# Performance work log

Measured on AMD Instinct MI355X. Metric: run time of the kernel, lower is better.

## Reference

```python
import jax, jax.numpy as jnp
import numpy as np

B, N, C, F, O = 32, 2048, 8, 128, 128


def setup_inputs() -> dict:
    key = jax.random.key(0)
    k1, k2, k3, k4, k5, k6 = jax.random.split(key, 6)
    nodes = jax.random.normal(k1, (B, N, F), dtype=jnp.float32)
    children = jax.random.randint(k2, (B, N, C), 0, N, dtype=jnp.int32)
    w_t = jax.random.normal(k3, (F, O), dtype=jnp.float32) * 0.05
    w_l = jax.random.normal(k4, (F, O), dtype=jnp.float32) * 0.05
    w_r = jax.random.normal(k5, (F, O), dtype=jnp.float32) * 0.05
    b = jax.random.normal(k6, (O,), dtype=jnp.float32) * 0.05
    return {"nodes": nodes, "children": children, "w_t": w_t, "w_l": w_l, "w_r": w_r, "b": b}


def reference(nodes, children, w_t, w_l, w_r, b):
    Bb, Nn, Ff = nodes.shape
    Cc = children.shape[2]
    dt = nodes.dtype

    # --- children tensor: index 0 maps to zero vector ---
    lookup = jnp.concatenate([jnp.zeros((Bb, 1, Ff), dt), nodes[:, 1:, :]], axis=1)
    batch_idx = jnp.arange(Bb)[:, None, None]
    child_vecs = lookup[batch_idx, children]                      # [B,N,C,F]
    tree = jnp.concatenate([nodes[:, :, None, :], child_vecs], axis=2)  # [B,N,C+1,F]

    # --- coefficients ---
    ch_f = children.astype(dt)
    c_t = jnp.broadcast_to(
        jnp.concatenate([jnp.ones((1, 1, 1), dt), jnp.zeros((1, 1, Cc), dt)], axis=2),
        (Bb, Nn, Cc + 1))                                          # [B,N,C+1]
    num_sib = jnp.count_nonzero(children, axis=2, keepdims=True).astype(dt)  # [B,N,1]
    mask = jnp.concatenate(
        [jnp.zeros((Bb, Nn, 1), dt), jnp.minimum(ch_f, 1.0)], axis=2)        # [B,N,C+1]
    child_indices = jnp.arange(-1.0, Cc, 1.0, dtype=dt)[None, None, :] * mask
    singles = jnp.concatenate(
        [jnp.zeros((Bb, Nn, 1), dt),
         jnp.full((Bb, Nn, 1), 0.5, dt),
         jnp.zeros((Bb, Nn, Cc - 1), dt)], axis=2)
    is_single = num_sib == 1.0
    denom = jnp.where(is_single, 1.0, num_sib - 1.0)  # safe divide, matches tf.where select
    c_r = jnp.where(is_single, singles, (1.0 - c_t) * (child_indices / denom))
    c_l = (1.0 - c_t) * (1.0 - c_r) * mask
    coef = jnp.stack([c_t, c_r, c_l], axis=3)                      # [B,N,C+1,3]

    # --- weighted aggregation + small GEMM ---
    agg = jnp.einsum('bncf,bnck->bnkf', tree, coef)                # [B,N,3,F]
    w = jnp.stack([w_t, w_r, w_l], axis=0)                         # [3,F,O]
    out = jnp.einsum('bnkf,kfo->bno', agg, w)
    return jax.nn.relu(out + b)
```

## Files before the change

### kernel.cpp

```cpp
#include <hip/hip_runtime.h>

typedef unsigned short ushort_t;
typedef __attribute__((ext_vector_type(8))) short short8;
typedef __attribute__((ext_vector_type(4))) short short4v;
typedef __attribute__((ext_vector_type(4))) float float4v;

#define Bn 32
#define Nn 2048
#define Cn 8
#define Fn 128
#define On 128
#define Kn 384
#define MT 16
#define LDSK 392

__device__ __forceinline__ ushort_t f2bf(float x) {
  unsigned u = __float_as_uint(x);
  u += 0x7fffu + ((u >> 16) & 1u);
  return (ushort_t)(u >> 16);
}

__global__ void prep_w_kernel(const float* __restrict__ w_t,
                              const float* __restrict__ w_l,
                              const float* __restrict__ w_r,
                              ushort_t* __restrict__ wsw) {
  int t = blockIdx.x * blockDim.x + threadIdx.x;
  if (t >= 6144) return;
  int lane = t & 63;
  int r = t >> 6;
  int ks = r % 12;
  int q = r / 12;
  int col = q * 16 + (lane & 15);
  int kbase = ((lane >> 4) * 8) + ks * 32;
  ushort_t* dst = wsw + (size_t)t * 8;
#pragma unroll
  for (int j = 0; j < 8; ++j) {
    int k = kbase + j;
    const float* src = (k < Fn) ? w_t : (k < 2 * Fn) ? w_r : w_l;
    int f = k & (Fn - 1);
    dst[j] = f2bf(src[f * On + col]);
  }
}

__global__ __launch_bounds__(128, 5)
void tree_conv_kernel(const float* __restrict__ nodes,
                      const int* __restrict__ children,
                      const ushort_t* __restrict__ wsw,
                      const float* __restrict__ bias,
                      float* __restrict__ out) {
  __shared__ __align__(16) ushort_t agg[MT * LDSK];

  const int tid = threadIdx.x;

  const int sb = ((blockIdx.x & 7) << 9) | (blockIdx.x >> 3);

  {
    const int grp = tid >> 5;
    const int ln = tid & 31;

    int4 ca[4], cb[4];
#pragma unroll
    for (int it = 0; it < 4; ++it) {
      const int g = sb * MT + it * 4 + grp;
      const int4* chv = (const int4*)(children + (size_t)g * Cn);
      ca[it] = chv[0];
      cb[it] = chv[1];
    }

#pragma unroll
    for (int it = 0; it < 4; ++it) {
      const int row = it * 4 + grp;
      const int g = sb * MT + row;
      const int base_row = g & ~(Nn - 1);

      int idx[Cn] = {ca[it].x, ca[it].y, ca[it].z, ca[it].w,
                     cb[it].x, cb[it].y, cb[it].z, cb[it].w};

      int ns = 0;
#pragma unroll
      for (int c = 0; c < Cn; ++c) ns += (idx[c] != 0);
      const float denom = (ns > 1) ? (float)(ns - 1) : 1.0f;

      float crv[Cn], clv[Cn];
#pragma unroll
      for (int c = 0; c < Cn; ++c) {
        float m = (idx[c] != 0) ? 1.0f : 0.0f;
        float cr0 = (ns == 1) ? ((c == 0) ? 0.5f : 0.0f) : ((float)c / denom);
        float cr = cr0 * m;
        crv[c] = cr;
        clv[c] = (1.0f - cr) * m;
        idx[c] &= (Nn - 1);
      }

      const float4v sv = *((const float4v*)(nodes + (size_t)g * Fn) + ln);

      float4v rr = {0.f, 0.f, 0.f, 0.f};
      float4v ll = {0.f, 0.f, 0.f, 0.f};
#pragma unroll
      for (int c = 0; c < Cn; ++c) {
        const float4v v =
            *((const float4v*)(nodes + (size_t)(base_row + idx[c]) * Fn) + ln);
        rr += crv[c] * v;
        ll += clv[c] * v;
      }

      ushort_t* arow = agg + row * LDSK;
      short4v ps = {(short)f2bf(sv.x), (short)f2bf(sv.y),
                    (short)f2bf(sv.z), (short)f2bf(sv.w)};
      short4v pr = {(short)f2bf(rr.x), (short)f2bf(rr.y),
                    (short)f2bf(rr.z), (short)f2bf(rr.w)};
      short4v pl = {(short)f2bf(ll.x), (short)f2bf(ll.y),
                    (short)f2bf(ll.z), (short)f2bf(ll.w)};
      *(short4v*)(arow + ln * 4) = ps;
      *(short4v*)(arow + Fn + ln * 4) = pr;
      *(short4v*)(arow + 2 * Fn + ln * 4) = pl;
    }
  }

  __syncthreads();

  const int lane = tid & 63;
  const int wave = tid >> 6;
  const int l15 = lane & 15;
  const int quad = lane >> 4;

#pragma unroll
  for (int ct = 0; ct < 4; ++ct) {
    const int q = wave * 4 + ct;
    const short8* bp = (const short8*)wsw + (q * 12) * 64 + lane;
    short8 bfrag[12];
#pragma unroll
    for (int ks = 0; ks < 12; ++ks) bfrag[ks] = bp[ks * 64];

    const int col = q * 16 + l15;
    const float bb = bias[col];

    const ushort_t* ar = agg + l15 * LDSK + quad * 8;
    float4v acc = {0.f, 0.f, 0.f, 0.f};
#pragma unroll
    for (int ks = 0; ks < 12; ++ks) {
      short8 af = *(const short8*)(ar + ks * 32);
      acc = __builtin_amdgcn_mfma_f32_16x16x32_bf16(af, bfrag[ks], acc, 0, 0, 0);
    }
    const int grow0 = sb * MT + quad * 4;
#pragma unroll
    for (int r2 = 0; r2 < 4; ++r2) {
      out[(size_t)(grow0 + r2) * On + col] = fmaxf(acc[r2] + bb, 0.f);
    }
  }
}

extern "C" void kernel_launch(void* const* d_in, const int* in_sizes, int n_in,
                              void* d_out, int out_size, void* d_ws, size_t ws_size,
                              hipStream_t stream) {
  const float* nodes = (const float*)d_in[0];
  const int* children = (const int*)d_in[1];
  const float* w_t = (const float*)d_in[2];
  const float* w_l = (const float*)d_in[3];
  const float* w_r = (const float*)d_in[4];
  const float* bias = (const float*)d_in[5];
  float* out = (float*)d_out;
  ushort_t* wsw = (ushort_t*)d_ws;

  prep_w_kernel<<<24, 256, 0, stream>>>(w_t, w_l, w_r, wsw);
  tree_conv_kernel<<<(Bn * Nn) / MT, 128, 0, stream>>>(nodes, children, wsw, bias, out);
}
```

Baseline: 113.0 us.

## Software-pipeline gather rows, prefetch weight fragments, use packed bf16 conversion

The gather phase now issues the nine node loads for the next row before computing the current one, with two register buffers. Weight fragments for two column tiles are loaded before the barrier and the next ones are prefetched during the MFMA chains. The A fragments are read from LDS once and reused. Conversion uses v_cvt_pk_bf16_f32, and the left-coefficient sum is computed algebraically as the masked sum minus the right sum. Launch bounds drop from 5 to 3 blocks per CU, trading occupancy for more registers in flight.

```diff
diff --git a/kernel.cpp b/kernel.cpp
--- a/kernel.cpp
+++ b/kernel.cpp
@@ -2,8 +2,8 @@
 
 typedef unsigned short ushort_t;
 typedef __attribute__((ext_vector_type(8))) short short8;
-typedef __attribute__((ext_vector_type(4))) short short4v;
 typedef __attribute__((ext_vector_type(4))) float float4v;
+typedef __attribute__((ext_vector_type(2))) unsigned int uint2v;
 
 #define Bn 32
 #define Nn 2048
@@ -18,6 +18,19 @@
   unsigned u = __float_as_uint(x);
   u += 0x7fffu + ((u >> 16) & 1u);
   return (ushort_t)(u >> 16);
+}
+
+__device__ __forceinline__ unsigned cvt_pk_bf16(float lo, float hi) {
+  unsigned r;
+  asm("v_cvt_pk_bf16_f32 %0, %1, %2" : "=v"(r) : "v"(lo), "v"(hi));
+  return r;
+}
+
+__device__ __forceinline__ uint2v pack4(float4v v) {
+  uint2v r;
+  r.x = cvt_pk_bf16(v.x, v.y);
+  r.y = cvt_pk_bf16(v.z, v.w);
+  return r;
 }
 
 __global__ void prep_w_kernel(const float* __restrict__ w_t,
@@ -42,7 +55,68 @@
   }
 }
 
-__global__ __launch_bounds__(128, 5)
+__device__ __forceinline__ void issue_row(const float* __restrict__ nodes,
+                                          int sb, int grp, int ln,
+                                          const int4& a, const int4& b,
+                                          int it, float4v (&dst)[9]) {
+  const int row = it * 4 + grp;
+  const int g = sb * MT + row;
+  const int base_row = g & ~(Nn - 1);
+  const float4v* np = (const float4v*)nodes;
+  dst[0] = np[(size_t)g * (Fn / 4) + ln];
+  const int id[Cn] = {a.x, a.y, a.z, a.w, b.x, b.y, b.z, b.w};
+#pragma unroll
+  for (int c = 0; c < Cn; ++c) {
+    const int ix = id[c] & (Nn - 1);
+    dst[1 + c] = np[(size_t)(base_row + ix) * (Fn / 4) + ln];
+  }
+}
+
+__device__ __forceinline__ void compute_row(ushort_t* __restrict__ agg,
+                                            int grp, int ln,
+                                            const int4& a, const int4& b,
+                                            int it, const float4v (&v)[9]) {
+  const int row = it * 4 + grp;
+  const int id[Cn] = {a.x, a.y, a.z, a.w, b.x, b.y, b.z, b.w};
+  int ns = 0;
+#pragma unroll
+  for (int c = 0; c < Cn; ++c) ns += (id[c] != 0) ? 1 : 0;
+  const bool single = (ns == 1);
+  const float rden = (ns > 1) ? (1.0f / (float)(ns - 1)) : 0.0f;
+
+  float4v rr = {0.f, 0.f, 0.f, 0.f};
+  float4v ms = {0.f, 0.f, 0.f, 0.f};
+#pragma unroll
+  for (int c = 0; c < Cn; ++c) {
+    const float m = (id[c] != 0) ? 1.0f : 0.0f;
+    float cr = single ? ((c == 0) ? 0.5f : 0.0f) : ((float)c * rden);
+    cr *= m;
+    const float4v vc = v[1 + c];
+    rr += cr * vc;
+    ms += m * vc;
+  }
+  const float4v ll = ms - rr;
+
+  ushort_t* arow = agg + row * LDSK + ln * 4;
+  *(uint2v*)(arow)           = pack4(v[0]);
+  *(uint2v*)(arow + Fn)      = pack4(rr);
+  *(uint2v*)(arow + 2 * Fn)  = pack4(ll);
+}
+
+__device__ __forceinline__ void store_ct(float* __restrict__ out,
+                                         const float* __restrict__ bias,
+                                         int sb, int l15, int quad, int q,
+                                         const float4v& acc) {
+  const int col = q * 16 + l15;
+  const float bb = bias[col];
+  const int grow0 = sb * MT + quad * 4;
+#pragma unroll
+  for (int r2 = 0; r2 < 4; ++r2) {
+    out[(size_t)(grow0 + r2) * On + col] = fmaxf(acc[r2] + bb, 0.f);
+  }
+}
+
+__global__ __launch_bounds__(128, 3)
 void tree_conv_kernel(const float* __restrict__ nodes,
                       const int* __restrict__ children,
                       const ushort_t* __restrict__ wsw,
@@ -67,87 +141,67 @@
       cb[it] = chv[1];
     }
 
-#pragma unroll
-    for (int it = 0; it < 4; ++it) {
-      const int row = it * 4 + grp;
-      const int g = sb * MT + row;
-      const int base_row = g & ~(Nn - 1);
-
-      int idx[Cn] = {ca[it].x, ca[it].y, ca[it].z, ca[it].w,
-                     cb[it].x, cb[it].y, cb[it].z, cb[it].w};
-
-      int ns = 0;
-#pragma unroll
-      for (int c = 0; c < Cn; ++c) ns += (idx[c] != 0);
-      const float denom = (ns > 1) ? (float)(ns - 1) : 1.0f;
-
-      float crv[Cn], clv[Cn];
-#pragma unroll
-      for (int c = 0; c < Cn; ++c) {
-        float m = (idx[c] != 0) ? 1.0f : 0.0f;
-        float cr0 = (ns == 1) ? ((c == 0) ? 0.5f : 0.0f) : ((float)c / denom);
-        float cr = cr0 * m;
-        crv[c] = cr;
-        clv[c] = (1.0f - cr) * m;
-        idx[c] &= (Nn - 1);
-      }
-
-      const float4v sv = *((const float4v*)(nodes + (size_t)g * Fn) + ln);
-
-      float4v rr = {0.f, 0.f, 0.f, 0.f};
-      float4v ll = {0.f, 0.f, 0.f, 0.f};
-#pragma unroll
-      for (int c = 0; c < Cn; ++c) {
-        const float4v v =
-            *((const float4v*)(nodes + (size_t)(base_row + idx[c]) * Fn) + ln);
-        rr += crv[c] * v;
-        ll += clv[c] * v;
-      }
-
-      ushort_t* arow = agg + row * LDSK;
-      short4v ps = {(short)f2bf(sv.x), (short)f2bf(sv.y),
-                    (short)f2bf(sv.z), (short)f2bf(sv.w)};
-      short4v pr = {(short)f2bf(rr.x), (short)f2bf(rr.y),
-                    (short)f2bf(rr.z), (short)f2bf(rr.w)};
-      short4v pl = {(short)f2bf(ll.x), (short)f2bf(ll.y),
-                    (short)f2bf(ll.z), (short)f2bf(ll.w)};
-      *(short4v*)(arow + ln * 4) = ps;
-      *(short4v*)(arow + Fn + ln * 4) = pr;
-      *(short4v*)(arow + 2 * Fn + ln * 4) = pl;
-    }
-  }
-
-  __syncthreads();
+    float4v v0[9], v1[9];
+    issue_row(nodes, sb, grp, ln, ca[0], cb[0], 0, v0);
+    issue_row(nodes, sb, grp, ln, ca[1], cb[1], 1, v1);
+    compute_row(agg, grp, ln, ca[0], cb[0], 0, v0);
+    issue_row(nodes, sb, grp, ln, ca[2], cb[2], 2, v0);
+    compute_row(agg, grp, ln, ca[1], cb[1], 1, v1);
+    issue_row(nodes, sb, grp, ln, ca[3], cb[3], 3, v1);
+    compute_row(agg, grp, ln, ca[2], cb[2], 2, v0);
+    compute_row(agg, grp, ln, ca[3], cb[3], 3, v1);
+  }
 
   const int lane = tid & 63;
   const int wave = tid >> 6;
   const int l15 = lane & 15;
   const int quad = lane >> 4;
 
-#pragma unroll
-  for (int ct = 0; ct < 4; ++ct) {
-    const int q = wave * 4 + ct;
-    const short8* bp = (const short8*)wsw + (q * 12) * 64 + lane;
-    short8 bfrag[12];
-#pragma unroll
-    for (int ks = 0; ks < 12; ++ks) bfrag[ks] = bp[ks * 64];
-
-    const int col = q * 16 + l15;
-    const float bb = bias[col];
-
-    const ushort_t* ar = agg + l15 * LDSK + quad * 8;
-    float4v acc = {0.f, 0.f, 0.f, 0.f};
-#pragma unroll
-    for (int ks = 0; ks < 12; ++ks) {
-      short8 af = *(const short8*)(ar + ks * 32);
-      acc = __builtin_amdgcn_mfma_f32_16x16x32_bf16(af, bfrag[ks], acc, 0, 0, 0);
-    }
-    const int grow0 = sb * MT + quad * 4;
-#pragma unroll
-    for (int r2 = 0; r2 < 4; ++r2) {
-      out[(size_t)(grow0 + r2) * On + col] = fmaxf(acc[r2] + bb, 0.f);
-    }
-  }
+  short8 bf0[12], bf1[12];
+  const short8* bbase = (const short8*)wsw + lane;
+#pragma unroll
+  for (int ks = 0; ks < 12; ++ks) bf0[ks] = bbase[((wave * 4 + 0) * 12 + ks) * 64];
+#pragma unroll
+  for (int ks = 0; ks < 12; ++ks) bf1[ks] = bbase[((wave * 4 + 1) * 12 + ks) * 64];
+
+  asm volatile("s_waitcnt lgkmcnt(0)" ::: "memory");
+  __builtin_amdgcn_s_barrier();
+  asm volatile("" ::: "memory");
+
+  const ushort_t* ar = agg + l15 * LDSK + quad * 8;
+  short8 af[12];
+#pragma unroll
+  for (int ks = 0; ks < 12; ++ks) af[ks] = *(const short8*)(ar + ks * 32);
+
+  float4v acc;
+
+  acc = (float4v){0.f, 0.f, 0.f, 0.f};
+#pragma unroll
+  for (int ks = 0; ks < 12; ++ks)
+    acc = __builtin_amdgcn_mfma_f32_16x16x32_bf16(af[ks], bf0[ks], acc, 0, 0, 0);
+#pragma unroll
+  for (int ks = 0; ks < 12; ++ks) bf0[ks] = bbase[((wave * 4 + 2) * 12 + ks) * 64];
+  store_ct(out, bias, sb, l15, quad, wave * 4 + 0, acc);
+
+  acc = (float4v){0.f, 0.f, 0.f, 0.f};
+#pragma unroll
+  for (int ks = 0; ks < 12; ++ks)
+    acc = __builtin_amdgcn_mfma_f32_16x16x32_bf16(af[ks], bf1[ks], acc, 0, 0, 0);
+#pragma unroll
+  for (int ks = 0; ks < 12; ++ks) bf1[ks] = bbase[((wave * 4 + 3) * 12 + ks) * 64];
+  store_ct(out, bias, sb, l15, quad, wave * 4 + 1, acc);
+
+  acc = (float4v){0.f, 0.f, 0.f, 0.f};
+#pragma unroll
+  for (int ks = 0; ks < 12; ++ks)
+    acc = __builtin_amdgcn_mfma_f32_16x16x32_bf16(af[ks], bf0[ks], acc, 0, 0, 0);
+  store_ct(out, bias, sb, l15, quad, wave * 4 + 2, acc);
+
+  acc = (float4v){0.f, 0.f, 0.f, 0.f};
+#pragma unroll
+  for (int ks = 0; ks < 12; ++ks)
+    acc = __builtin_amdgcn_mfma_f32_16x16x32_bf16(af[ks], bf1[ks], acc, 0, 0, 0);
+  store_ct(out, bias, sb, l15, quad, wave * 4 + 3, acc);
 }
 
 extern "C" void kernel_launch(void* const* d_in, const int* in_sizes, int n_in,
```

Measured after the change: 119.9 us. +6.1%, slower.

## Stage bf16 node features in LDS per feature slice and gather children from shared memory

Applied to the files above, without the earlier changes.

A prep pass converts all node features to bf16 in workspace. Each 512-thread block then handles 256 rows of one batch and loops over four 32-feature slices. For each slice it loads the whole batch's 2048-node slice into swizzled LDS, gathers children from LDS, and accumulates MFMA results across slices. This replaces random fp32 global gathers with LDS gathers and computes the left coefficient as mask-sum minus right. The cost is an extra full conversion pass over nodes, and each block re-reads its whole batch, eight times per batch overall.

```diff
diff --git a/kernel.cpp b/kernel.cpp
--- a/kernel.cpp
+++ b/kernel.cpp
@@ -2,7 +2,6 @@
 
 typedef unsigned short ushort_t;
 typedef __attribute__((ext_vector_type(8))) short short8;
-typedef __attribute__((ext_vector_type(4))) short short4v;
 typedef __attribute__((ext_vector_type(4))) float float4v;
 
 #define Bn 32
@@ -10,9 +9,9 @@
 #define Cn 8
 #define Fn 128
 #define On 128
-#define Kn 384
-#define MT 16
-#define LDSK 392
+#define RPB 256
+#define NBLK ((Bn * Nn) / RPB)
+#define NBF_OFF 131072
 
 __device__ __forceinline__ ushort_t f2bf(float x) {
   unsigned u = __float_as_uint(x);
@@ -20,132 +19,191 @@
   return (ushort_t)(u >> 16);
 }
 
-__global__ void prep_w_kernel(const float* __restrict__ w_t,
-                              const float* __restrict__ w_l,
-                              const float* __restrict__ w_r,
-                              ushort_t* __restrict__ wsw) {
-  int t = blockIdx.x * blockDim.x + threadIdx.x;
-  if (t >= 6144) return;
-  int lane = t & 63;
-  int r = t >> 6;
-  int ks = r % 12;
-  int q = r / 12;
-  int col = q * 16 + (lane & 15);
-  int kbase = ((lane >> 4) * 8) + ks * 32;
-  ushort_t* dst = wsw + (size_t)t * 8;
-#pragma unroll
-  for (int j = 0; j < 8; ++j) {
-    int k = kbase + j;
-    const float* src = (k < Fn) ? w_t : (k < 2 * Fn) ? w_r : w_l;
-    int f = k & (Fn - 1);
-    dst[j] = f2bf(src[f * On + col]);
-  }
-}
-
-__global__ __launch_bounds__(128, 5)
-void tree_conv_kernel(const float* __restrict__ nodes,
+__device__ __forceinline__ unsigned cvt_pk_bf16(float lo, float hi) {
+  unsigned r;
+  asm("v_cvt_pk_bf16_f32 %0, %1, %2" : "=v"(r) : "v"(lo), "v"(hi));
+  return r;
+}
+
+__global__ void prep_kernel(const float* __restrict__ nodes,
+                            const float* __restrict__ w_t,
+                            const float* __restrict__ w_l,
+                            const float* __restrict__ w_r,
+                            ushort_t* __restrict__ wsw,
+                            ushort_t* __restrict__ nbf) {
+  if (blockIdx.x < 4096) {
+    const int t = blockIdx.x * 256 + threadIdx.x;
+    const float4v* s = (const float4v*)(nodes + (size_t)t * 8);
+    float4v a = s[0], b = s[1];
+    short8 d;
+    unsigned* du = (unsigned*)&d;
+    du[0] = cvt_pk_bf16(a.x, a.y);
+    du[1] = cvt_pk_bf16(a.z, a.w);
+    du[2] = cvt_pk_bf16(b.x, b.y);
+    du[3] = cvt_pk_bf16(b.z, b.w);
+    *(short8*)(nbf + (size_t)t * 8) = d;
+  } else {
+    const int t = (blockIdx.x - 4096) * 256 + threadIdx.x;
+    if (t >= 6144) return;
+    const int lane = t & 63;
+    const int r = t >> 6;
+    const int ks = r % 12;
+    const int q = r / 12;
+    const int col = q * 16 + (lane & 15);
+    const int kbase = ((lane >> 4) * 8) + ks * 32;
+    ushort_t* dst = wsw + (size_t)t * 8;
+#pragma unroll
+    for (int j = 0; j < 8; ++j) {
+      const int k = kbase + j;
+      const float* src = (k < Fn) ? w_t : (k < 2 * Fn) ? w_r : w_l;
+      const int f = k & (Fn - 1);
+      dst[j] = f2bf(src[f * On + col]);
+    }
+  }
+}
+
+__device__ __forceinline__ void gather_tile(const ushort_t* __restrict__ nds,
+                                            int selfad, const int (&cad)[Cn],
+                                            const float (&crv)[Cn],
+                                            const float (&mv)[Cn],
+                                            short8& aft, short8& afr,
+                                            short8& afl) {
+  aft = *(const short8*)(nds + selfad);
+  float rr[8] = {0, 0, 0, 0, 0, 0, 0, 0};
+  float ms[8] = {0, 0, 0, 0, 0, 0, 0, 0};
+#pragma unroll
+  for (int c = 0; c < Cn; ++c) {
+    const short8 cv = *(const short8*)(nds + cad[c]);
+    const unsigned* u = (const unsigned*)&cv;
+    float f[8];
+#pragma unroll
+    for (int p = 0; p < 4; ++p) {
+      f[2 * p]     = __uint_as_float(u[p] << 16);
+      f[2 * p + 1] = __uint_as_float(u[p] & 0xffff0000u);
+    }
+    const float cr = crv[c], m = mv[c];
+#pragma unroll
+    for (int j = 0; j < 8; ++j) {
+      rr[j] += cr * f[j];
+      ms[j] += m * f[j];
+    }
+  }
+  unsigned* pr = (unsigned*)&afr;
+  unsigned* pl = (unsigned*)&afl;
+#pragma unroll
+  for (int p = 0; p < 4; ++p) {
+    pr[p] = cvt_pk_bf16(rr[2 * p], rr[2 * p + 1]);
+    pl[p] = cvt_pk_bf16(ms[2 * p] - rr[2 * p], ms[2 * p + 1] - rr[2 * p + 1]);
+  }
+}
+
+__global__ __launch_bounds__(512, 2)
+void tree_conv_kernel(const ushort_t* __restrict__ nbf,
                       const int* __restrict__ children,
                       const ushort_t* __restrict__ wsw,
                       const float* __restrict__ bias,
                       float* __restrict__ out) {
-  __shared__ __align__(16) ushort_t agg[MT * LDSK];
+  __shared__ __align__(16) ushort_t nds[Nn * 32];
 
   const int tid = threadIdx.x;
-
-  const int sb = ((blockIdx.x & 7) << 9) | (blockIdx.x >> 3);
-
-  {
-    const int grp = tid >> 5;
-    const int ln = tid & 31;
-
-    int4 ca[4], cb[4];
-#pragma unroll
-    for (int it = 0; it < 4; ++it) {
-      const int g = sb * MT + it * 4 + grp;
-      const int4* chv = (const int4*)(children + (size_t)g * Cn);
-      ca[it] = chv[0];
-      cb[it] = chv[1];
-    }
-
-#pragma unroll
-    for (int it = 0; it < 4; ++it) {
-      const int row = it * 4 + grp;
-      const int g = sb * MT + row;
-      const int base_row = g & ~(Nn - 1);
-
-      int idx[Cn] = {ca[it].x, ca[it].y, ca[it].z, ca[it].w,
-                     cb[it].x, cb[it].y, cb[it].z, cb[it].w};
-
-      int ns = 0;
-#pragma unroll
-      for (int c = 0; c < Cn; ++c) ns += (idx[c] != 0);
-      const float denom = (ns > 1) ? (float)(ns - 1) : 1.0f;
-
-      float crv[Cn], clv[Cn];
-#pragma unroll
-      for (int c = 0; c < Cn; ++c) {
-        float m = (idx[c] != 0) ? 1.0f : 0.0f;
-        float cr0 = (ns == 1) ? ((c == 0) ? 0.5f : 0.0f) : ((float)c / denom);
-        float cr = cr0 * m;
-        crv[c] = cr;
-        clv[c] = (1.0f - cr) * m;
-        idx[c] &= (Nn - 1);
-      }
-
-      const float4v sv = *((const float4v*)(nodes + (size_t)g * Fn) + ln);
-
-      float4v rr = {0.f, 0.f, 0.f, 0.f};
-      float4v ll = {0.f, 0.f, 0.f, 0.f};
-#pragma unroll
-      for (int c = 0; c < Cn; ++c) {
-        const float4v v =
-            *((const float4v*)(nodes + (size_t)(base_row + idx[c]) * Fn) + ln);
-        rr += crv[c] * v;
-        ll += clv[c] * v;
-      }
-
-      ushort_t* arow = agg + row * LDSK;
-      short4v ps = {(short)f2bf(sv.x), (short)f2bf(sv.y),
-                    (short)f2bf(sv.z), (short)f2bf(sv.w)};
-      short4v pr = {(short)f2bf(rr.x), (short)f2bf(rr.y),
-                    (short)f2bf(rr.z), (short)f2bf(rr.w)};
-      short4v pl = {(short)f2bf(ll.x), (short)f2bf(ll.y),
-                    (short)f2bf(ll.z), (short)f2bf(ll.w)};
-      *(short4v*)(arow + ln * 4) = ps;
-      *(short4v*)(arow + Fn + ln * 4) = pr;
-      *(short4v*)(arow + 2 * Fn + ln * 4) = pl;
-    }
-  }
-
-  __syncthreads();
-
-  const int lane = tid & 63;
-  const int wave = tid >> 6;
-  const int l15 = lane & 15;
-  const int quad = lane >> 4;
-
-#pragma unroll
-  for (int ct = 0; ct < 4; ++ct) {
-    const int q = wave * 4 + ct;
-    const short8* bp = (const short8*)wsw + (q * 12) * 64 + lane;
-    short8 bfrag[12];
-#pragma unroll
-    for (int ks = 0; ks < 12; ++ks) bfrag[ks] = bp[ks * 64];
-
-    const int col = q * 16 + l15;
-    const float bb = bias[col];
-
-    const ushort_t* ar = agg + l15 * LDSK + quad * 8;
-    float4v acc = {0.f, 0.f, 0.f, 0.f};
-#pragma unroll
-    for (int ks = 0; ks < 12; ++ks) {
-      short8 af = *(const short8*)(ar + ks * 32);
-      acc = __builtin_amdgcn_mfma_f32_16x16x32_bf16(af, bfrag[ks], acc, 0, 0, 0);
-    }
-    const int grow0 = sb * MT + quad * 4;
-#pragma unroll
-    for (int r2 = 0; r2 < 4; ++r2) {
-      out[(size_t)(grow0 + r2) * On + col] = fmaxf(acc[r2] + bb, 0.f);
+  const int sblk = ((blockIdx.x & 7) << 5) | (blockIdx.x >> 3);
+  const int batch = sblk >> 3;
+  const int row0 = (sblk & 7) * RPB;
+
+  const int ln = tid & 63;
+  const int wv = tid >> 6;
+  const int l15 = ln & 15;
+  const int quad = ln >> 4;
+
+  const ushort_t* nb = nbf + (size_t)batch * (Nn * Fn);
+
+  int cad[2][Cn], selfad[2];
+  float crv[2][Cn], mv[2][Cn];
+#pragma unroll
+  for (int t2 = 0; t2 < 2; ++t2) {
+    const int brow = row0 + (wv * 2 + t2) * 16 + l15;
+    const int4* p4 = (const int4*)(children + ((size_t)batch * Nn + brow) * Cn);
+    const int4 a = p4[0], b = p4[1];
+    const int id[Cn] = {a.x, a.y, a.z, a.w, b.x, b.y, b.z, b.w};
+    int ns = 0;
+#pragma unroll
+    for (int c = 0; c < Cn; ++c) ns += (id[c] != 0) ? 1 : 0;
+    const bool single = (ns == 1);
+    const float rden = (ns > 1) ? (1.0f / (float)(ns - 1)) : 0.0f;
+#pragma unroll
+    for (int c = 0; c < Cn; ++c) {
+      const float m = (id[c] != 0) ? 1.0f : 0.0f;
+      const float cr = single ? ((c == 0) ? 0.5f : 0.0f) : ((float)c * rden);
+      crv[t2][c] = cr * m;
+      mv[t2][c] = m;
+      const int ix = id[c] & (Nn - 1);
+      cad[t2][c] = ix * 32 + ((quad ^ (ix & 3)) * 8);
+    }
+    selfad[t2] = brow * 32 + ((quad ^ (brow & 3)) * 8);
+  }
+  float bb[8];
+#pragma unroll
+  for (int q = 0; q < 8; ++q) bb[q] = bias[q * 16 + l15];
+
+  float4v acc[2][8];
+#pragma unroll
+  for (int t2 = 0; t2 < 2; ++t2)
+#pragma unroll
+    for (int q = 0; q < 8; ++q) acc[t2][q] = (float4v){0.f, 0.f, 0.f, 0.f};
+
+  const short8* wb = (const short8*)wsw + ln;
+
+  for (int ph = 0; ph < 4; ++ph) {
+    if (ph) __syncthreads();
+
+    {
+      short8 tmp[16];
+#pragma unroll
+      for (int i = 0; i < 16; ++i) {
+        const int idx = i * 512 + tid;
+        const int r = idx >> 2;
+        const int ch = idx & 3;
+        tmp[i] = *(const short8*)(nb + (size_t)r * Fn + ph * 32 + ch * 8);
+      }
+#pragma unroll
+      for (int i = 0; i < 16; ++i) {
+        const int idx = i * 512 + tid;
+        const int r = idx >> 2;
+        const int ch = idx & 3;
+        *(short8*)(nds + r * 32 + ((ch ^ (r & 3)) * 8)) = tmp[i];
+      }
+    }
+    __syncthreads();
+
+    short8 af[2][3];
+#pragma unroll
+    for (int t2 = 0; t2 < 2; ++t2)
+      gather_tile(nds, selfad[t2], cad[t2], crv[t2], mv[t2],
+                  af[t2][0], af[t2][1], af[t2][2]);
+
+#pragma unroll
+    for (int kind = 0; kind < 3; ++kind) {
+#pragma unroll
+      for (int q = 0; q < 8; ++q) {
+        const short8 b = wb[(q * 12 + kind * 4 + ph) * 64];
+        acc[0][q] = __builtin_amdgcn_mfma_f32_16x16x32_bf16(af[0][kind], b,
+                                                            acc[0][q], 0, 0, 0);
+        acc[1][q] = __builtin_amdgcn_mfma_f32_16x16x32_bf16(af[1][kind], b,
+                                                            acc[1][q], 0, 0, 0);
+      }
+    }
+  }
+
+#pragma unroll
+  for (int t2 = 0; t2 < 2; ++t2) {
+    const int grow0 = batch * Nn + row0 + (wv * 2 + t2) * 16 + quad * 4;
+#pragma unroll
+    for (int q = 0; q < 8; ++q) {
+#pragma unroll
+      for (int r2 = 0; r2 < 4; ++r2) {
+        out[(size_t)(grow0 + r2) * On + q * 16 + l15] =
+            fmaxf(acc[t2][q][r2] + bb[q], 0.f);
+      }
     }
   }
 }
@@ -161,7 +219,8 @@
   const float* bias = (const float*)d_in[5];
   float* out = (float*)d_out;
   ushort_t* wsw = (ushort_t*)d_ws;
-
-  prep_w_kernel<<<24, 256, 0, stream>>>(w_t, w_l, w_r, wsw);
-  tree_conv_kernel<<<(Bn * Nn) / MT, 128, 0, stream>>>(nodes, children, wsw, bias, out);
-}
+  ushort_t* nbf = (ushort_t*)((char*)d_ws + NBF_OFF);
+
+  prep_kernel<<<4120, 256, 0, stream>>>(nodes, w_t, w_l, w_r, wsw, nbf);
+  tree_conv_kernel<<<NBLK, 512, 0, stream>>>(nbf, children, wsw, bias, out);
+}
```

New measurement: 134.2 us. 18.7% more time.
